# Kernel tuning notes

Hardware: AMD Instinct MI355X
Metric: run time of the kernel (lower is better)

The kernel has to match this reference:

```python
import jax, jax.numpy as jnp
import numpy as np

N, D, DEG, DEPTH, H = 50000, 300, 6, 3, 4
E = N * DEG
DK = D // H


def setup_inputs() -> dict:
    key = jax.random.key(0)
    ks = jax.random.split(key, 14)
    # circulant molecular-like graph: node i <-> i+k (k=1,2,3), edges emitted in
    # reverse pairs (2t, 2t+1) as required by reverse_edge()
    u = np.arange(N)
    src_l, dst_l = [], []
    for k in (1, 2, 3):
        v = (u + k) % N
        src_l.append(np.stack([u, v], 1).reshape(-1))
        dst_l.append(np.stack([v, u], 1).reshape(-1))
    src = np.concatenate(src_l).astype(np.int32)
    dst = np.concatenate(dst_l).astype(np.int32)
    # incoming-edge ids per node (every node has exactly DEG in-edges)
    order = np.argsort(dst, kind='stable')
    nbr_eids = order.reshape(N, DEG).astype(np.int32)
    nbr_mask = np.ones((N, DEG), dtype=bool)
    sd = 1.0 / np.sqrt(D)
    p = lambda i, shape: jax.random.normal(ks[i], shape, jnp.float32) * sd
    return {
        'f': jax.random.normal(ks[0], (N, D), jnp.float32),
        'x': jax.random.normal(ks[1], (E, D), jnp.float32),
        'Wq': p(2, (D, D)), 'bq': jnp.zeros((D,), jnp.float32),
        'Wk': p(3, (D, D)), 'bk': jnp.zeros((D,), jnp.float32),
        'Wv': p(4, (D, D)), 'bv': jnp.zeros((D,), jnp.float32),
        'Wo': p(5, (D, D)), 'bo': jnp.zeros((D,), jnp.float32),
        'W_mp': p(6, (DEPTH - 1, D, D)), 'b_mp': jnp.zeros((DEPTH - 1, D), jnp.float32),
        'W_last': p(7, (3 * D, D)), 'b_last': jnp.zeros((D,), jnp.float32),
        'src': jnp.asarray(src), 'dst': jnp.asarray(dst),
        'nbr_eids': jnp.asarray(nbr_eids), 'nbr_mask': jnp.asarray(nbr_mask),
    }


def reference(f, x, Wq, bq, Wk, bk, Wv, bv, Wo, bo, W_mp, b_mp, W_last, b_last,
              src, dst, nbr_eids, nbr_mask):
    n = f.shape[0]
    e = x.shape[0]
    rev = jnp.arange(e) ^ 1                     # reverse-pair permutation
    has_in = nbr_mask.any(axis=-1)              # [N]
    scale = 1.0 / jnp.sqrt(jnp.float32(DK))
    h = x                                       # edge state 'h' init from 'x'
    f_h = f                                     # node state 'f_h' init from 'f'
    for i in range(DEPTH - 1):
        # ragged mailbox of incoming edge states, padded to DEG
        m = jnp.where(nbr_mask[..., None], h[nbr_eids], 0.0)        # [N,DEG,D]
        q = (f_h @ Wq + bq).reshape(n, H, DK)                        # query = node feat
        k = (m @ Wk + bk).reshape(n, DEG, H, DK)                     # key   = mailbox
        v = ((m + f_h[:, None, :]) @ Wv + bv).reshape(n, DEG, H, DK) # value = mailbox + feat
        scores = jnp.einsum('nhk,ndhk->nhd', q, k) * scale          # [N,H,DEG]
        scores = jnp.where(nbr_mask[:, None, :], scores, -1e9)
        attn = jax.nn.softmax(scores, axis=-1)
        out = jnp.einsum('nhd,ndhk->nhk', attn, v).reshape(n, D) @ Wo + bo
        f_h = jnp.where(has_in[:, None], out, f_h)
        # edge update: m = f_h[src] - rev_h; h = relu(x + Linear_i(m))
        m_e = f_h[src] - h[rev]
        h = jax.nn.relu(x + m_e @ W_mp[i] + b_mp[i])
    # GEANet is undefined in the provided source -> identity pass-through
    mail = jax.ops.segment_sum(h, dst, num_segments=n)              # sum of in-edge states
    f_new = jnp.concatenate([mail, f_h, f], axis=-1) @ W_last + b_last
    f_final = jnp.where(has_in[:, None], f_new, f_h)
    return f_final, h
```

## Files before the change

### kernel.cpp

```cpp
#include <hip/hip_runtime.h>
#include <hip/hip_bf16.h>

typedef unsigned long long ull;
typedef unsigned int u32;
typedef unsigned short u16;
typedef __hip_bfloat16 bf16;
typedef __attribute__((ext_vector_type(8))) short v8s;
typedef __attribute__((ext_vector_type(4))) float v4f;
typedef __attribute__((ext_vector_type(2))) ull v2u;

#define NN 50000
#define DD 300
#define PD 320
#define EE (NN*6)

__device__ __forceinline__ u16 f2bf(float f) {
    u32 u = __float_as_uint(f);
    u32 r = u + 0x7FFFu + ((u >> 16) & 1u);
    return (u16)(r >> 16);
}
__device__ __forceinline__ u32 cvtpk(float lo, float hi) {
    u32 r;
    asm("v_cvt_pk_bf16_f32 %0, %1, %2" : "=v"(r) : "v"(lo), "v"(hi));
    return r;
}
__device__ __forceinline__ float lo16(u32 u) { return __uint_as_float(u << 16); }
__device__ __forceinline__ float hi16(u32 u) { return __uint_as_float(u & 0xffff0000u); }

__device__ __forceinline__ void gl16(const void* g, void* l) {
    __builtin_amdgcn_global_load_lds(
        (const __attribute__((address_space(1))) u32*)g,
        (__attribute__((address_space(3))) u32*)l, 16, 0, 0);
}

enum { E_BIAS = 0, E_RELUX = 1 };
enum { O_F32 = 1, O_BF16 = 2 };
enum { GM_LIN = 0, GM_SRC = 1, GM_REV = 2 };

template<int EPI, int OUTM, int NW, int NSEG>
__global__ __launch_bounds__(NW*64)
void gemm_mfma(const bf16* __restrict__ A0, const bf16* __restrict__ A1,
               const bf16* __restrict__ A2, const bf16* __restrict__ A3,
               const bf16* __restrict__ A4,
               const int* __restrict__ srcidx, int gmodes,
               const bf16* __restrict__ BT,
               const float* __restrict__ bias0, const float* __restrict__ bias1,
               const bf16* __restrict__ xepi,
               float* __restrict__ Cf, bf16* __restrict__ Cb0, bf16* __restrict__ Cb1,
               int M, int ybias, long ycb)
{
    __shared__ __align__(16) char Als[64 * 640];
    const int tid = threadIdx.x;
    const int wave = tid >> 6, lane = tid & 63;
    const int l15 = lane & 15, l4 = lane >> 4;
    const int wv = (NW == 8) ? (wave & 3) : wave;
    const int half = (NW == 8) ? (wave >> 2) : 0;
    const int rowBase = blockIdx.x * 64;
    const int T = NW * 64;
    const int gy = blockIdx.y;
    BT += (long)gy * 204800;
    if (bias0) bias0 += (long)gy * ybias;
    if (bias1) bias1 += (long)gy * ybias;
    if (Cb0) Cb0 += gy * ycb;
    if (Cb1) Cb1 += gy * ycb;

    v4f acc[4][5];
    const v4f vzero = {0.f, 0.f, 0.f, 0.f};
    #pragma unroll
    for (int mt = 0; mt < 4; ++mt)
        #pragma unroll
        for (int nt = 0; nt < 5; ++nt) acc[mt][nt] = vzero;

    for (int seg = 0; seg < NSEG; ++seg) {
        const bf16* As = (seg == 0) ? A0 : (seg == 1 ? A1 : (seg == 2 ? A2 :
                         (seg == 3 ? A3 : A4)));
        const int gm = (gmodes >> (seg * 3)) & 7;
        if (seg) __syncthreads();
        #pragma unroll
        for (int s = 0; s < 2560 / T; ++s) {
            int c = tid + T * s;
            int r = c / 40, ch = c - r * 40;
            int gc = rowBase + r;
            gc = (gc < M) ? gc : (M - 1);
            int row = (gm == GM_SRC) ? srcidx[gc] :
                      ((gm == GM_REV) ? (gc ^ 1) : gc);
            int chs = ((ch * 16) ^ ((r & 7) << 4)) >> 4;
            int lbase = (c - lane) * 16;
            gl16(As + (long)row * PD + chs * 8, Als + lbase);
        }
        __syncthreads();

        const bf16* BTs = BT + (long)seg * 320 * PD;
        #pragma unroll
        for (int ks = 0; ks < 10; ++ks) {
            v8s af[4];
            #pragma unroll
            for (int mt = 0; mt < 4; ++mt) {
                int rowL = mt * 16 + l15;
                af[mt] = *(const v8s*)(Als +
                    ((rowL * 640 + ks * 64 + l4 * 16) ^ ((rowL & 7) << 4)));
            }
            #pragma unroll
            for (int nt = 0; nt < 5; ++nt) {
                int col = wave * 80 + nt * 16 + l15;
                v8s bfr = *(const v8s*)(BTs + (long)col * PD + ks * 32 + l4 * 8);
                #pragma unroll
                for (int mt = 0; mt < 4; ++mt)
                    acc[mt][nt] = __builtin_amdgcn_mfma_f32_16x16x32_bf16(
                        af[mt], bfr, acc[mt][nt], 0, 0, 0);
            }
        }
    }

    const int NOUT = (NW == 8) ? 2 : 1;
    #pragma unroll
    for (int oh = 0; oh < NOUT; ++oh) {
        __syncthreads();
        if (half == oh) {
            const float* bias = oh ? bias1 : bias0;
            #pragma unroll
            for (int nt = 0; nt < 5; ++nt) {
                int col = wv * 80 + nt * 16 + l15;
                float bvv = bias ? bias[col] : 0.f;
                #pragma unroll
                for (int mt = 0; mt < 4; ++mt) {
                    #pragma unroll
                    for (int r = 0; r < 4; ++r) {
                        int rowL = mt * 16 + l4 * 4 + r;
                        *(u16*)(Als + ((rowL * 640 + col * 2) ^ (((rowL >> 2) & 7) << 4)))
                            = f2bf(acc[mt][nt][r] + bvv);
                    }
                }
            }
        }
        __syncthreads();
        {
            bf16* Cb = oh ? Cb1 : Cb0;
            #pragma unroll
            for (int s = 0; s < 2560 / T; ++s) {
                int c = tid + T * s;
                int r = c / 40, ch = c - r * 40;
                int grow = rowBase + r;
                if (grow >= M) continue;
                v2u val = *(const v2u*)(Als + ((c * 16) ^ (((r >> 2) & 7) << 4)));
                if (EPI == E_RELUX) {
                    v2u xv = *(const v2u*)(xepi + (long)grow * PD + ch * 8);
                    #pragma unroll
                    for (int w = 0; w < 2; ++w) {
                        u32 a0 = (u32)val[w], a1 = (u32)(val[w] >> 32);
                        u32 x0 = (u32)xv[w],  x1 = (u32)(xv[w] >> 32);
                        u32 r0 = cvtpk(fmaxf(lo16(a0) + lo16(x0), 0.f),
                                       fmaxf(hi16(a0) + hi16(x0), 0.f));
                        u32 r1 = cvtpk(fmaxf(lo16(a1) + lo16(x1), 0.f),
                                       fmaxf(hi16(a1) + hi16(x1), 0.f));
                        val[w] = (ull)r0 | ((ull)r1 << 32);
                    }
                }
                if (OUTM & O_BF16)
                    *(v2u*)(Cb + (long)grow * PD + ch * 8) = val;
                if (OUTM & O_F32) {
                    int col0 = ch * 8;
                    if (col0 < DD) {
                        u32 a0 = (u32)val[0], a1 = (u32)(val[0] >> 32);
                        float4 lo = {lo16(a0), hi16(a0), lo16(a1), hi16(a1)};
                        *(float4*)(Cf + (long)grow * DD + col0) = lo;
                        if (col0 + 4 < DD) {
                            u32 b0 = (u32)val[1], b1 = (u32)(val[1] >> 32);
                            float4 hi = {lo16(b0), hi16(b0), lo16(b1), hi16(b1)};
                            *(float4*)(Cf + (long)grow * DD + col0 + 4) = hi;
                        }
                    }
                }
            }
        }
    }
}

__global__ __launch_bounds__(256)
void scoreU_k(const bf16* __restrict__ G0, const bf16* __restrict__ G1,
              const bf16* __restrict__ G2, const bf16* __restrict__ G3,
              const bf16* __restrict__ h, const int* __restrict__ nbr,
              bf16* __restrict__ U0, bf16* __restrict__ U1,
              bf16* __restrict__ U2, bf16* __restrict__ U3)
{
    int wave = threadIdx.x >> 6, lane = threadIdx.x & 63;
    int n = blockIdx.x * 4 + wave;
    if (n >= NN) return;
    int eid[6];
    #pragma unroll
    for (int d = 0; d < 6; ++d) eid[d] = nbr[n * 6 + d];

    bool act = lane < 40;
    int cl = act ? lane : 0;
    long go = (long)n * PD + cl * 8;

    float g[4][8];
    #pragma unroll
    for (int hh = 0; hh < 4; ++hh) {
        const bf16* Gp = (hh == 0) ? G0 : (hh == 1) ? G1 : (hh == 2) ? G2 : G3;
        v2u gv = *(const v2u*)(Gp + go);
        u32 w0 = (u32)gv[0], w1 = (u32)(gv[0] >> 32);
        u32 w2 = (u32)gv[1], w3 = (u32)(gv[1] >> 32);
        g[hh][0] = lo16(w0); g[hh][1] = hi16(w0);
        g[hh][2] = lo16(w1); g[hh][3] = hi16(w1);
        g[hh][4] = lo16(w2); g[hh][5] = hi16(w2);
        g[hh][6] = lo16(w3); g[hh][7] = hi16(w3);
        if (!act)
            #pragma unroll
            for (int i = 0; i < 8; ++i) g[hh][i] = 0.f;
    }
    v2u hp[6];
    #pragma unroll
    for (int d = 0; d < 6; ++d)
        hp[d] = *(const v2u*)(h + (long)eid[d] * PD + cl * 8);

    float s0[6], s1[6], s2[6], s3[6];
    #pragma unroll
    for (int d = 0; d < 6; ++d) {
        u32 w0 = (u32)hp[d][0], w1 = (u32)(hp[d][0] >> 32);
        u32 w2 = (u32)hp[d][1], w3 = (u32)(hp[d][1] >> 32);
        float hf[8] = {lo16(w0), hi16(w0), lo16(w1), hi16(w1),
                       lo16(w2), hi16(w2), lo16(w3), hi16(w3)};
        float p0 = 0, p1 = 0, p2 = 0, p3 = 0;
        #pragma unroll
        for (int i = 0; i < 8; ++i) {
            p0 += g[0][i] * hf[i];
            p1 += g[1][i] * hf[i];
            p2 += g[2][i] * hf[i];
            p3 += g[3][i] * hf[i];
        }
        #pragma unroll
        for (int off = 32; off; off >>= 1) {
            p0 += __shfl_xor(p0, off);
            p1 += __shfl_xor(p1, off);
            p2 += __shfl_xor(p2, off);
            p3 += __shfl_xor(p3, off);
        }
        s0[d] = p0; s1[d] = p1; s2[d] = p2; s3[d] = p3;
    }

    const float scale = 0.1154700538379252f;
    float at[4][6];
    {
        float m0 = -1e30f, m1 = -1e30f, m2 = -1e30f, m3 = -1e30f;
        #pragma unroll
        for (int d = 0; d < 6; ++d) {
            s0[d] *= scale; s1[d] *= scale; s2[d] *= scale; s3[d] *= scale;
            m0 = fmaxf(m0, s0[d]); m1 = fmaxf(m1, s1[d]);
            m2 = fmaxf(m2, s2[d]); m3 = fmaxf(m3, s3[d]);
        }
        float t0 = 0, t1 = 0, t2 = 0, t3 = 0;
        #pragma unroll
        for (int d = 0; d < 6; ++d) {
            at[0][d] = expf(s0[d] - m0); t0 += at[0][d];
            at[1][d] = expf(s1[d] - m1); t1 += at[1][d];
            at[2][d] = expf(s2[d] - m2); t2 += at[2][d];
            at[3][d] = expf(s3[d] - m3); t3 += at[3][d];
        }
        t0 = 1.f / t0; t1 = 1.f / t1; t2 = 1.f / t2; t3 = 1.f / t3;
        #pragma unroll
        for (int d = 0; d < 6; ++d) {
            at[0][d] *= t0; at[1][d] *= t1; at[2][d] *= t2; at[3][d] *= t3;
        }
    }

    float u[4][8];
    #pragma unroll
    for (int hh = 0; hh < 4; ++hh)
        #pragma unroll
        for (int i = 0; i < 8; ++i) u[hh][i] = 0.f;
    #pragma unroll
    for (int d = 0; d < 6; ++d) {
        u32 w0 = (u32)hp[d][0], w1 = (u32)(hp[d][0] >> 32);
        u32 w2 = (u32)hp[d][1], w3 = (u32)(hp[d][1] >> 32);
        float hf[8] = {lo16(w0), hi16(w0), lo16(w1), hi16(w1),
                       lo16(w2), hi16(w2), lo16(w3), hi16(w3)};
        #pragma unroll
        for (int i = 0; i < 8; ++i) {
            u[0][i] += at[0][d] * hf[i];
            u[1][i] += at[1][d] * hf[i];
            u[2][i] += at[2][d] * hf[i];
            u[3][i] += at[3][d] * hf[i];
        }
    }
    if (act) {
        #pragma unroll
        for (int hh = 0; hh < 4; ++hh) {
            bf16* Up = (hh == 0) ? U0 : (hh == 1) ? U1 : (hh == 2) ? U2 : U3;
            v2u r;
            r[0] = (ull)cvtpk(u[hh][0], u[hh][1]) |
                   ((ull)cvtpk(u[hh][2], u[hh][3]) << 32);
            r[1] = (ull)cvtpk(u[hh][4], u[hh][5]) |
                   ((ull)cvtpk(u[hh][6], u[hh][7]) << 32);
            *(v2u*)(Up + go) = r;
        }
    }
}

__global__ __launch_bounds__(256)
void mailf_k(const float* __restrict__ h, const int* __restrict__ nbr,
             bf16* __restrict__ mail)
{
    int idx = blockIdx.x * 256 + threadIdx.x;
    if (idx >= NN * 80) return;
    int n = idx / 80, c4 = idx - n * 80;
    float4 s = {0.f, 0.f, 0.f, 0.f};
    if (c4 < 75) {
        const int* e = nbr + n * 6;
        #pragma unroll
        for (int d = 0; d < 6; ++d) {
            float4 v = *(const float4*)(h + (long)e[d] * DD + c4 * 4);
            s.x += v.x; s.y += v.y; s.z += v.z; s.w += v.w;
        }
    }
    ull r = (ull)cvtpk(s.x, s.y) | ((ull)cvtpk(s.z, s.w) << 32);
    *(ull*)(mail + (long)n * PD + c4 * 4) = r;
}

__global__ __launch_bounds__(256)
void conv_k(const float* __restrict__ in, bf16* __restrict__ out, int rows)
{
    long idx = (long)blockIdx.x * 256 + threadIdx.x;
    if (idx >= (long)rows * 40) return;
    int r = (int)(idx / 40), ch = (int)(idx - (long)r * 40);
    int c4 = ch * 2;
    float4 a = {0, 0, 0, 0}, b = {0, 0, 0, 0};
    if (c4 < 75)     a = *(const float4*)(in + (long)r * DD + c4 * 4);
    if (c4 + 1 < 75) b = *(const float4*)(in + (long)r * DD + c4 * 4 + 4);
    v2u v;
    v[0] = (ull)cvtpk(a.x, a.y) | ((ull)cvtpk(a.z, a.w) << 32);
    v[1] = (ull)cvtpk(b.x, b.y) | ((ull)cvtpk(b.z, b.w) << 32);
    *(v2u*)(out + (long)r * PD + ch * 8) = v;
}

__global__ __launch_bounds__(256)
void tw_k(const float* __restrict__ W, bf16* __restrict__ BT, float sgn)
{
    int idx = blockIdx.x * 256 + threadIdx.x;
    if (idx >= 320 * 320) return;
    int nn = idx / 320, kk = idx - nn * 320;
    u16 v = 0;
    if (nn < DD && kk < DD) v = f2bf(sgn * W[kk * DD + nn]);
    ((u16*)BT)[idx] = v;
}

__global__ __launch_bounds__(256)
void twf_k(const float* __restrict__ W, float* __restrict__ WT)
{
    __shared__ float t[32][33];
    int bx = blockIdx.x % 10, by = blockIdx.x / 10;
    int r0 = by * 32, c0 = bx * 32;
    int tx = threadIdx.x & 31, ty = threadIdx.x >> 5;
    #pragma unroll
    for (int i = 0; i < 4; ++i) {
        int r = r0 + ty + i * 8, c = c0 + tx;
        t[ty + i * 8][tx] = (r < DD && c < DD) ? W[r * DD + c] : 0.f;
    }
    __syncthreads();
    #pragma unroll
    for (int i = 0; i < 4; ++i)
        WT[(c0 + ty + i * 8) * 320 + r0 + tx] = t[tx][ty + i * 8];
}

__global__ __launch_bounds__(256)
void wqk_k(const float* __restrict__ WqT, const float* __restrict__ Wk,
           bf16* __restrict__ slab)
{
    int idx = blockIdx.x * 256 + threadIdx.x;
    if (idx >= 1280 * 320) return;
    int c = idx / 320, k = idx - c * 320;
    int hh = c / 320;
    int ci = c - hh * 320;
    float v = 0.f;
    if (ci < DD && k < DD) {
        int jb = hh * 75;
        for (int j = 0; j < 75; ++j)
            v += WqT[(jb + j) * 320 + k] * Wk[ci * DD + jb + j];
    }
    ((u16*)slab)[idx] = f2bf(v);
}

__global__ __launch_bounds__(256)
void wcomp_k(const float* __restrict__ WvT, const float* __restrict__ Wo,
             bf16* __restrict__ slab)
{
    int idx = blockIdx.x * 256 + threadIdx.x;
    if (idx >= 5 * 320 * 320) return;
    int s = idx / 102400, rem = idx - s * 102400;
    int c = rem / 320, k = rem - c * 320;
    float v = 0.f;
    if (c < DD && k < DD) {
        int jb = (s < 4) ? s * 75 : 0;
        int jn = (s < 4) ? 75 : 300;
        for (int j = 0; j < jn; ++j)
            v += WvT[(jb + j) * 320 + k] * Wo[(jb + j) * DD + c];
    }
    ((u16*)slab)[idx] = f2bf(v);
}

__global__ void bias_k(const float* __restrict__ WkT, const float* __restrict__ Wo,
                       const float* __restrict__ bq, const float* __restrict__ bv,
                       const float* __restrict__ bo, const float* __restrict__ bmp,
                       const float* __restrict__ blast, float* __restrict__ outb)
{
    int a = blockIdx.x, i = threadIdx.x;
    float v = 0.f;
    if (i < DD) {
        if (a < 4) {
            for (int j = 0; j < 75; ++j)
                v += bq[a * 75 + j] * WkT[(a * 75 + j) * 320 + i];
        } else if (a == 4) {
            for (int j = 0; j < DD; ++j) v += bv[j] * Wo[j * DD + i];
            v += bo[i];
        } else if (a == 5) v = bmp[i];
        else if (a == 6) v = bmp[DD + i];
        else v = blast[i];
    }
    outb[a * 320 + i] = v;
}

extern "C" void kernel_launch(void* const* d_in, const int* in_sizes, int n_in,
                              void* d_out, int out_size, void* d_ws, size_t ws_size,
                              hipStream_t stream)
{
    const float* f     = (const float*)d_in[0];
    const float* x     = (const float*)d_in[1];
    const float* Wq    = (const float*)d_in[2];
    const float* bq    = (const float*)d_in[3];
    const float* Wk    = (const float*)d_in[4];
    const float* bv    = (const float*)d_in[7];
    const float* Wv    = (const float*)d_in[6];
    const float* Wo    = (const float*)d_in[8];
    const float* bo    = (const float*)d_in[9];
    const float* Wmp   = (const float*)d_in[10];
    const float* bmp   = (const float*)d_in[11];
    const float* Wlast = (const float*)d_in[12];
    const float* blast = (const float*)d_in[13];
    const int*   src   = (const int*)d_in[14];
    const int*   nbr   = (const int*)d_in[16];

    float* out     = (float*)d_out;
    float* f_final = out;
    float* h_final = out + (long)NN * DD;

    char* ws = (char*)d_ws;
    bf16* xb  = (bf16*)(ws);
    bf16* h1b = (bf16*)(ws + 192000000LL);
    bf16* fb  = (bf16*)(ws + 576000000LL);
    bf16* G0  = (bf16*)(ws + 608000000LL);
    bf16* G1  = (bf16*)(ws + 640000000LL);
    bf16* G2  = (bf16*)(ws + 672000000LL);
    bf16* G3  = (bf16*)(ws + 704000000LL);
    bf16* FHb = (bf16*)(ws + 736000000LL);
    bf16* WT  = (bf16*)(ws + 768000000LL);
    float* BIAS = (float*)(ws + 771300000LL);
    float* WqT  = (float*)(ws + 771400000LL);
    float* WkT  = (float*)(ws + 771850000LL);
    float* WvT  = (float*)(ws + 772300000LL);
    auto slot = [&](int i) { return WT + (long)i * 320 * 320; };
    bf16* qk   = slot(0);
    bf16* fh5  = slot(4);
    float* g0p = BIAS;          float* g1p = BIAS + 320;
    float* b2p = BIAS + 1280;
    float* bm0p = BIAS + 1600;  float* bm1p = BIAS + 1920;
    float* blp = BIAS + 2240;
    bf16* MLb = G0;

    dim3 blk(256), blk8(512);
    const int gN = (NN + 63) / 64;
    const int gE = (EE + 63) / 64;

    conv_k<<<(int)(((long)EE * 40 + 255) / 256), blk, 0, stream>>>(x, xb, EE);
    conv_k<<<(int)(((long)NN * 40 + 255) / 256), blk, 0, stream>>>(f, fb, NN);
    twf_k<<<100, blk, 0, stream>>>(Wq, WqT);
    twf_k<<<100, blk, 0, stream>>>(Wk, WkT);
    twf_k<<<100, blk, 0, stream>>>(Wv, WvT);
    wqk_k<<<1600, blk, 0, stream>>>(WqT, Wk, qk);
    wcomp_k<<<2000, blk, 0, stream>>>(WvT, Wo, fh5);
    tw_k<<<400, blk, 0, stream>>>(Wmp, slot(9), 1.f);
    tw_k<<<400, blk, 0, stream>>>(Wmp, slot(10), -1.f);
    tw_k<<<400, blk, 0, stream>>>(Wmp + 90000, slot(11), 1.f);
    tw_k<<<400, blk, 0, stream>>>(Wmp + 90000, slot(12), -1.f);
    tw_k<<<400, blk, 0, stream>>>(Wlast, slot(13), 1.f);
    tw_k<<<400, blk, 0, stream>>>(Wlast + 90000, slot(14), 1.f);
    tw_k<<<400, blk, 0, stream>>>(Wlast + 180000, slot(15), 1.f);
    bias_k<<<8, 320, 0, stream>>>(WkT, Wo, bq, bv, bo, bmp, blast, BIAS);

    const int GM_MP = GM_SRC | (GM_REV << 3);

    for (int it = 0; it < 2; ++it) {
        const bf16* hb  = it ? h1b : xb;
        const bf16* fhb = it ? FHb : fb;
        gemm_mfma<E_BIAS, O_BF16, 8, 1><<<dim3(gN, 2), blk8, 0, stream>>>(
            fhb, nullptr, nullptr, nullptr, nullptr, nullptr, 0, qk,
            g0p, g1p, nullptr, nullptr, G0, G1, NN, 640, 32000000);
        scoreU_k<<<(NN + 3) / 4, blk, 0, stream>>>(G0, G1, G2, G3, hb, nbr,
                                                   G0, G1, G2, G3);
        gemm_mfma<E_BIAS, O_BF16, 4, 5><<<gN, blk, 0, stream>>>(
            G0, G1, G2, G3, fhb, nullptr, 0, fh5, b2p, nullptr, nullptr,
            nullptr, FHb, nullptr, NN, 0, 0);
        if (it == 0) {
            gemm_mfma<E_RELUX, O_BF16, 4, 2><<<gE, blk, 0, stream>>>(
                FHb, hb, nullptr, nullptr, nullptr, src, GM_MP, slot(9),
                bm0p, nullptr, xb, nullptr, h1b, nullptr, EE, 0, 0);
        } else {
            gemm_mfma<E_RELUX, O_F32, 4, 2><<<gE, blk, 0, stream>>>(
                FHb, hb, nullptr, nullptr, nullptr, src, GM_MP, slot(11),
                bm1p, nullptr, xb, h_final, nullptr, nullptr, EE, 0, 0);
        }
    }

    mailf_k<<<(NN * 80 + 255) / 256, blk, 0, stream>>>(h_final, nbr, MLb);
    gemm_mfma<E_BIAS, O_F32, 4, 3><<<gN, blk, 0, stream>>>(
        MLb, FHb, fb, nullptr, nullptr, nullptr, 0, slot(13), blp, nullptr,
        nullptr, f_final, nullptr, nullptr, NN, 0, 0);
}
```

Measured before the change: 2.606 ms.

## Precompute node-side message GEMM and use reverse-edge linearity in edge GEMM

The edge update (f_h[src] - h[rev]) @ W is split algebraically. f_h @ W + b is computed once per node by a small GEMM, and the edge GEMM now multiplies only h @ W. In the epilogue it gathers the node product by src and takes the reverse-pair row (r^1) of its own tile from LDS. This removes a full K=320 segment and the src-gather from the large E-row GEMM. All GEMMs move to a 512-thread, 2x4 wave tiling with 2x5 accumulators per wave, and the QK GEMM splits into 4 y-slices. The extra node GEMM and an extra bf16 rounding of both partial products are the costs, and numerical error may differ slightly.

New measurement: 2.263 ms. 1.15x faster.

```diff
diff --git a/kernel.cpp b/kernel.cpp
--- a/kernel.cpp
+++ b/kernel.cpp
@@ -33,142 +33,147 @@
         (__attribute__((address_space(3))) u32*)l, 16, 0, 0);
 }
 
-enum { E_BIAS = 0, E_RELUX = 1 };
+enum { E_BIAS = 0, E_MPF = 1 };
 enum { O_F32 = 1, O_BF16 = 2 };
-enum { GM_LIN = 0, GM_SRC = 1, GM_REV = 2 };
-
-template<int EPI, int OUTM, int NW, int NSEG>
-__global__ __launch_bounds__(NW*64)
+
+template<int EPI, int OUTM, int NSEG>
+__global__ __launch_bounds__(512, 4)
 void gemm_mfma(const bf16* __restrict__ A0, const bf16* __restrict__ A1,
                const bf16* __restrict__ A2, const bf16* __restrict__ A3,
                const bf16* __restrict__ A4,
-               const int* __restrict__ srcidx, int gmodes,
-               const bf16* __restrict__ BT,
-               const float* __restrict__ bias0, const float* __restrict__ bias1,
+               const int* __restrict__ srcidx, const bf16* __restrict__ FHW,
+               const bf16* __restrict__ BT, const float* __restrict__ bias0,
                const bf16* __restrict__ xepi,
-               float* __restrict__ Cf, bf16* __restrict__ Cb0, bf16* __restrict__ Cb1,
-               int M, int ybias, long ycb)
+               float* __restrict__ Cf, bf16* __restrict__ Cb0,
+               int M, long ycb)
 {
     __shared__ __align__(16) char Als[64 * 640];
     const int tid = threadIdx.x;
     const int wave = tid >> 6, lane = tid & 63;
     const int l15 = lane & 15, l4 = lane >> 4;
-    const int wv = (NW == 8) ? (wave & 3) : wave;
-    const int half = (NW == 8) ? (wave >> 2) : 0;
+    const int wr = wave >> 2, wc = wave & 3;
     const int rowBase = blockIdx.x * 64;
-    const int T = NW * 64;
     const int gy = blockIdx.y;
-    BT += (long)gy * 204800;
-    if (bias0) bias0 += (long)gy * ybias;
-    if (bias1) bias1 += (long)gy * ybias;
-    if (Cb0) Cb0 += gy * ycb;
-    if (Cb1) Cb1 += gy * ycb;
-
-    v4f acc[4][5];
+    BT += (long)gy * 102400;
+    if (bias0) bias0 += (long)gy * 320;
+    if (Cb0) Cb0 += (long)gy * ycb;
+
+    v4f acc[2][5];
     const v4f vzero = {0.f, 0.f, 0.f, 0.f};
     #pragma unroll
-    for (int mt = 0; mt < 4; ++mt)
+    for (int mt = 0; mt < 2; ++mt)
         #pragma unroll
         for (int nt = 0; nt < 5; ++nt) acc[mt][nt] = vzero;
 
     for (int seg = 0; seg < NSEG; ++seg) {
         const bf16* As = (seg == 0) ? A0 : (seg == 1 ? A1 : (seg == 2 ? A2 :
                          (seg == 3 ? A3 : A4)));
-        const int gm = (gmodes >> (seg * 3)) & 7;
         if (seg) __syncthreads();
         #pragma unroll
-        for (int s = 0; s < 2560 / T; ++s) {
-            int c = tid + T * s;
+        for (int s = 0; s < 5; ++s) {
+            int c = tid + 512 * s;
             int r = c / 40, ch = c - r * 40;
-            int gc = rowBase + r;
-            gc = (gc < M) ? gc : (M - 1);
-            int row = (gm == GM_SRC) ? srcidx[gc] :
-                      ((gm == GM_REV) ? (gc ^ 1) : gc);
-            int chs = ((ch * 16) ^ ((r & 7) << 4)) >> 4;
-            int lbase = (c - lane) * 16;
-            gl16(As + (long)row * PD + chs * 8, Als + lbase);
+            int grow = rowBase + r;
+            grow = (grow < M) ? grow : (M - 1);
+            int chs = ch ^ (r & 7);
+            gl16(As + (long)grow * PD + chs * 8,
+                 Als + (wave * 64 + 512 * s) * 16);
         }
         __syncthreads();
 
-        const bf16* BTs = BT + (long)seg * 320 * PD;
+        const bf16* BTs = BT + (long)seg * 102400;
         #pragma unroll
         for (int ks = 0; ks < 10; ++ks) {
-            v8s af[4];
+            v8s af[2];
             #pragma unroll
-            for (int mt = 0; mt < 4; ++mt) {
-                int rowL = mt * 16 + l15;
+            for (int mt = 0; mt < 2; ++mt) {
+                int rowL = wr * 32 + mt * 16 + l15;
                 af[mt] = *(const v8s*)(Als +
                     ((rowL * 640 + ks * 64 + l4 * 16) ^ ((rowL & 7) << 4)));
             }
             #pragma unroll
             for (int nt = 0; nt < 5; ++nt) {
-                int col = wave * 80 + nt * 16 + l15;
+                int col = wc * 80 + nt * 16 + l15;
                 v8s bfr = *(const v8s*)(BTs + (long)col * PD + ks * 32 + l4 * 8);
                 #pragma unroll
-                for (int mt = 0; mt < 4; ++mt)
+                for (int mt = 0; mt < 2; ++mt)
                     acc[mt][nt] = __builtin_amdgcn_mfma_f32_16x16x32_bf16(
                         af[mt], bfr, acc[mt][nt], 0, 0, 0);
             }
         }
     }
 
-    const int NOUT = (NW == 8) ? 2 : 1;
-    #pragma unroll
-    for (int oh = 0; oh < NOUT; ++oh) {
-        __syncthreads();
-        if (half == oh) {
-            const float* bias = oh ? bias1 : bias0;
+    __syncthreads();
+    #pragma unroll
+    for (int nt = 0; nt < 5; ++nt) {
+        int col = wc * 80 + nt * 16 + l15;
+        float bvv = bias0 ? bias0[col] : 0.f;
+        #pragma unroll
+        for (int mt = 0; mt < 2; ++mt) {
             #pragma unroll
-            for (int nt = 0; nt < 5; ++nt) {
-                int col = wv * 80 + nt * 16 + l15;
-                float bvv = bias ? bias[col] : 0.f;
-                #pragma unroll
-                for (int mt = 0; mt < 4; ++mt) {
-                    #pragma unroll
-                    for (int r = 0; r < 4; ++r) {
-                        int rowL = mt * 16 + l4 * 4 + r;
-                        *(u16*)(Als + ((rowL * 640 + col * 2) ^ (((rowL >> 2) & 7) << 4)))
-                            = f2bf(acc[mt][nt][r] + bvv);
+            for (int rr = 0; rr < 4; ++rr) {
+                int rowL = wr * 32 + mt * 16 + l4 * 4 + rr;
+                *(u16*)(Als + ((rowL * 640 + col * 2) ^ (((rowL >> 2) & 7) << 4)))
+                    = f2bf(acc[mt][nt][rr] + bvv);
+            }
+        }
+    }
+    __syncthreads();
+
+    #pragma unroll
+    for (int s = 0; s < 5; ++s) {
+        int c = tid + 512 * s;
+        int r = c / 40, ch = c - r * 40;
+        int grow = rowBase + r;
+        if (grow >= M) continue;
+        if (EPI == E_MPF) {
+            v2u hv = *(const v2u*)(Als +
+                (((r ^ 1) * 640 + ch * 16) ^ (((r >> 2) & 7) << 4)));
+            v2u xv = *(const v2u*)(xepi + (long)grow * PD + ch * 8);
+            int sr = srcidx[grow];
+            v2u fw = *(const v2u*)(FHW + (long)sr * PD + ch * 8);
+            float vf[8];
+            #pragma unroll
+            for (int w = 0; w < 2; ++w) {
+                u32 h0 = (u32)hv[w], h1 = (u32)(hv[w] >> 32);
+                u32 x0 = (u32)xv[w], x1 = (u32)(xv[w] >> 32);
+                u32 f0 = (u32)fw[w], f1 = (u32)(fw[w] >> 32);
+                vf[w*4+0] = fmaxf(lo16(x0) + lo16(f0) - lo16(h0), 0.f);
+                vf[w*4+1] = fmaxf(hi16(x0) + hi16(f0) - hi16(h0), 0.f);
+                vf[w*4+2] = fmaxf(lo16(x1) + lo16(f1) - lo16(h1), 0.f);
+                vf[w*4+3] = fmaxf(hi16(x1) + hi16(f1) - hi16(h1), 0.f);
+            }
+            if (OUTM & O_BF16) {
+                v2u rv;
+                rv[0] = (ull)cvtpk(vf[0], vf[1]) | ((ull)cvtpk(vf[2], vf[3]) << 32);
+                rv[1] = (ull)cvtpk(vf[4], vf[5]) | ((ull)cvtpk(vf[6], vf[7]) << 32);
+                *(v2u*)(Cb0 + (long)grow * PD + ch * 8) = rv;
+            }
+            if (OUTM & O_F32) {
+                int col0 = ch * 8;
+                if (col0 < DD) {
+                    float4 lo = {vf[0], vf[1], vf[2], vf[3]};
+                    *(float4*)(Cf + (long)grow * DD + col0) = lo;
+                    if (col0 + 4 < DD) {
+                        float4 hi4 = {vf[4], vf[5], vf[6], vf[7]};
+                        *(float4*)(Cf + (long)grow * DD + col0 + 4) = hi4;
                     }
                 }
             }
-        }
-        __syncthreads();
-        {
-            bf16* Cb = oh ? Cb1 : Cb0;
-            #pragma unroll
-            for (int s = 0; s < 2560 / T; ++s) {
-                int c = tid + T * s;
-                int r = c / 40, ch = c - r * 40;
-                int grow = rowBase + r;
-                if (grow >= M) continue;
-                v2u val = *(const v2u*)(Als + ((c * 16) ^ (((r >> 2) & 7) << 4)));
-                if (EPI == E_RELUX) {
-                    v2u xv = *(const v2u*)(xepi + (long)grow * PD + ch * 8);
-                    #pragma unroll
-                    for (int w = 0; w < 2; ++w) {
-                        u32 a0 = (u32)val[w], a1 = (u32)(val[w] >> 32);
-                        u32 x0 = (u32)xv[w],  x1 = (u32)(xv[w] >> 32);
-                        u32 r0 = cvtpk(fmaxf(lo16(a0) + lo16(x0), 0.f),
-                                       fmaxf(hi16(a0) + hi16(x0), 0.f));
-                        u32 r1 = cvtpk(fmaxf(lo16(a1) + lo16(x1), 0.f),
-                                       fmaxf(hi16(a1) + hi16(x1), 0.f));
-                        val[w] = (ull)r0 | ((ull)r1 << 32);
-                    }
-                }
-                if (OUTM & O_BF16)
-                    *(v2u*)(Cb + (long)grow * PD + ch * 8) = val;
-                if (OUTM & O_F32) {
-                    int col0 = ch * 8;
-                    if (col0 < DD) {
-                        u32 a0 = (u32)val[0], a1 = (u32)(val[0] >> 32);
-                        float4 lo = {lo16(a0), hi16(a0), lo16(a1), hi16(a1)};
-                        *(float4*)(Cf + (long)grow * DD + col0) = lo;
-                        if (col0 + 4 < DD) {
-                            u32 b0 = (u32)val[1], b1 = (u32)(val[1] >> 32);
-                            float4 hi = {lo16(b0), hi16(b0), lo16(b1), hi16(b1)};
-                            *(float4*)(Cf + (long)grow * DD + col0 + 4) = hi;
-                        }
+        } else {
+            v2u val = *(const v2u*)(Als + ((c * 16) ^ (((r >> 2) & 7) << 4)));
+            if (OUTM & O_BF16)
+                *(v2u*)(Cb0 + (long)grow * PD + ch * 8) = val;
+            if (OUTM & O_F32) {
+                int col0 = ch * 8;
+                if (col0 < DD) {
+                    u32 a0 = (u32)val[0], a1 = (u32)(val[0] >> 32);
+                    float4 lo = {lo16(a0), hi16(a0), lo16(a1), hi16(a1)};
+                    *(float4*)(Cf + (long)grow * DD + col0) = lo;
+                    if (col0 + 4 < DD) {
+                        u32 b0 = (u32)val[1], b1 = (u32)(val[1] >> 32);
+                        float4 hi4 = {lo16(b0), hi16(b0), lo16(b1), hi16(b1)};
+                        *(float4*)(Cf + (long)grow * DD + col0 + 4) = hi4;
                     }
                 }
             }
@@ -334,13 +339,13 @@
 }
 
 __global__ __launch_bounds__(256)
-void tw_k(const float* __restrict__ W, bf16* __restrict__ BT, float sgn)
+void tw_k(const float* __restrict__ W, bf16* __restrict__ BT)
 {
     int idx = blockIdx.x * 256 + threadIdx.x;
     if (idx >= 320 * 320) return;
     int nn = idx / 320, kk = idx - nn * 320;
     u16 v = 0;
-    if (nn < DD && kk < DD) v = f2bf(sgn * W[kk * DD + nn]);
+    if (nn < DD && kk < DD) v = f2bf(W[kk * DD + nn]);
     ((u16*)BT)[idx] = v;
 }
 
@@ -460,13 +465,14 @@
     auto slot = [&](int i) { return WT + (long)i * 320 * 320; };
     bf16* qk   = slot(0);
     bf16* fh5  = slot(4);
-    float* g0p = BIAS;          float* g1p = BIAS + 320;
+    float* g0p = BIAS;
     float* b2p = BIAS + 1280;
     float* bm0p = BIAS + 1600;  float* bm1p = BIAS + 1920;
     float* blp = BIAS + 2240;
     bf16* MLb = G0;
-
-    dim3 blk(256), blk8(512);
+    bf16* FHW = G1;
+
+    dim3 blk(256), blk5(512);
     const int gN = (NN + 63) / 64;
     const int gE = (EE + 63) / 64;
 
@@ -477,41 +483,42 @@
     twf_k<<<100, blk, 0, stream>>>(Wv, WvT);
     wqk_k<<<1600, blk, 0, stream>>>(WqT, Wk, qk);
     wcomp_k<<<2000, blk, 0, stream>>>(WvT, Wo, fh5);
-    tw_k<<<400, blk, 0, stream>>>(Wmp, slot(9), 1.f);
-    tw_k<<<400, blk, 0, stream>>>(Wmp, slot(10), -1.f);
-    tw_k<<<400, blk, 0, stream>>>(Wmp + 90000, slot(11), 1.f);
-    tw_k<<<400, blk, 0, stream>>>(Wmp + 90000, slot(12), -1.f);
-    tw_k<<<400, blk, 0, stream>>>(Wlast, slot(13), 1.f);
-    tw_k<<<400, blk, 0, stream>>>(Wlast + 90000, slot(14), 1.f);
-    tw_k<<<400, blk, 0, stream>>>(Wlast + 180000, slot(15), 1.f);
+    tw_k<<<400, blk, 0, stream>>>(Wmp, slot(9));
+    tw_k<<<400, blk, 0, stream>>>(Wmp + 90000, slot(10));
+    tw_k<<<400, blk, 0, stream>>>(Wlast, slot(11));
+    tw_k<<<400, blk, 0, stream>>>(Wlast + 90000, slot(12));
+    tw_k<<<400, blk, 0, stream>>>(Wlast + 180000, slot(13));
     bias_k<<<8, 320, 0, stream>>>(WkT, Wo, bq, bv, bo, bmp, blast, BIAS);
-
-    const int GM_MP = GM_SRC | (GM_REV << 3);
 
     for (int it = 0; it < 2; ++it) {
         const bf16* hb  = it ? h1b : xb;
         const bf16* fhb = it ? FHb : fb;
-        gemm_mfma<E_BIAS, O_BF16, 8, 1><<<dim3(gN, 2), blk8, 0, stream>>>(
-            fhb, nullptr, nullptr, nullptr, nullptr, nullptr, 0, qk,
-            g0p, g1p, nullptr, nullptr, G0, G1, NN, 640, 32000000);
+        const bf16* mpW = it ? slot(10) : slot(9);
+        const float* bmP = it ? bm1p : bm0p;
+        gemm_mfma<E_BIAS, O_BF16, 1><<<dim3(gN, 4), blk5, 0, stream>>>(
+            fhb, nullptr, nullptr, nullptr, nullptr, nullptr, nullptr,
+            qk, g0p, nullptr, nullptr, G0, NN, 16000000);
         scoreU_k<<<(NN + 3) / 4, blk, 0, stream>>>(G0, G1, G2, G3, hb, nbr,
                                                    G0, G1, G2, G3);
-        gemm_mfma<E_BIAS, O_BF16, 4, 5><<<gN, blk, 0, stream>>>(
-            G0, G1, G2, G3, fhb, nullptr, 0, fh5, b2p, nullptr, nullptr,
-            nullptr, FHb, nullptr, NN, 0, 0);
+        gemm_mfma<E_BIAS, O_BF16, 5><<<gN, blk5, 0, stream>>>(
+            G0, G1, G2, G3, fhb, nullptr, nullptr, fh5, b2p, nullptr,
+            nullptr, FHb, NN, 0);
+        gemm_mfma<E_BIAS, O_BF16, 1><<<gN, blk5, 0, stream>>>(
+            FHb, nullptr, nullptr, nullptr, nullptr, nullptr, nullptr,
+            mpW, bmP, nullptr, nullptr, FHW, NN, 0);
         if (it == 0) {
-            gemm_mfma<E_RELUX, O_BF16, 4, 2><<<gE, blk, 0, stream>>>(
-                FHb, hb, nullptr, nullptr, nullptr, src, GM_MP, slot(9),
-                bm0p, nullptr, xb, nullptr, h1b, nullptr, EE, 0, 0);
+            gemm_mfma<E_MPF, O_BF16, 1><<<gE, blk5, 0, stream>>>(
+                hb, nullptr, nullptr, nullptr, nullptr, src, FHW,
+                mpW, nullptr, xb, nullptr, h1b, EE, 0);
         } else {
-            gemm_mfma<E_RELUX, O_F32, 4, 2><<<gE, blk, 0, stream>>>(
-                FHb, hb, nullptr, nullptr, nullptr, src, GM_MP, slot(11),
-                bm1p, nullptr, xb, h_final, nullptr, nullptr, EE, 0, 0);
+            gemm_mfma<E_MPF, O_F32, 1><<<gE, blk5, 0, stream>>>(
+                hb, nullptr, nullptr, nullptr, nullptr, src, FHW,
+                mpW, nullptr, xb, h_final, nullptr, EE, 0);
         }
     }
 
     mailf_k<<<(NN * 80 + 255) / 256, blk, 0, stream>>>(h_final, nbr, MLb);
-    gemm_mfma<E_BIAS, O_F32, 4, 3><<<gN, blk, 0, stream>>>(
-        MLb, FHb, fb, nullptr, nullptr, nullptr, 0, slot(13), blp, nullptr,
-        nullptr, f_final, nullptr, nullptr, NN, 0, 0);
-}
+    gemm_mfma<E_BIAS, O_F32, 3><<<gN, blk5, 0, stream>>>(
+        MLb, FHb, fb, nullptr, nullptr, nullptr, nullptr, slot(11), blp,
+        nullptr, f_final, nullptr, NN, 0);
+}
```
